# Kernel tuning notes

Hardware: AMD Instinct MI355X
Metric: run time of the kernel (lower is better)

Reference implementation:

```python
import jax, jax.numpy as jnp
import numpy as np

N, E, IN_C, HEADS, OUT_C = 50000, 800000, 256, 8, 32
NEG_SLOPE = 0.2
BN_EPS = 1e-5


def setup_inputs() -> dict:
    key = jax.random.key(0)
    ks = jax.random.split(key, 12)
    x = jax.random.normal(ks[0], (N, IN_C), jnp.float32)
    edge_index = jax.random.randint(ks[1], (2, E), 0, N, dtype=jnp.int32)
    edge_attr = jax.random.uniform(ks[2], (E, 1), jnp.float32)
    s = 0.1
    W = jax.random.normal(ks[3], (IN_C, HEADS * OUT_C), jnp.float32) * s
    att_src = jax.random.normal(ks[4], (HEADS, OUT_C), jnp.float32) * s
    att_dst = jax.random.normal(ks[5], (HEADS, OUT_C), jnp.float32) * s
    W_edge = jax.random.normal(ks[6], (1, HEADS * OUT_C), jnp.float32) * s
    att_edge = jax.random.normal(ks[7], (HEADS, OUT_C), jnp.float32) * s
    bias = jnp.zeros((HEADS * OUT_C,), jnp.float32)
    gamma = jnp.ones((HEADS * OUT_C,), jnp.float32)
    beta = jnp.zeros((HEADS * OUT_C,), jnp.float32)
    return {"x": x, "edge_index": edge_index, "edge_attr": edge_attr, "W": W,
            "att_src": att_src, "att_dst": att_dst, "W_edge": W_edge,
            "att_edge": att_edge, "bias": bias, "gamma": gamma, "beta": beta}


def reference(x, edge_index, edge_attr, W, att_src, att_dst, W_edge, att_edge, bias, gamma, beta):
    # --- add self loops (fill_value='mean' for edge_attr, PyG GATConv default) ---
    loops = jnp.arange(N, dtype=edge_index.dtype)
    src = jnp.concatenate([edge_index[0], loops])      # [E+N]
    dst = jnp.concatenate([edge_index[1], loops])      # [E+N]
    ea_mean = jnp.mean(edge_attr, axis=0, keepdims=True)
    ea = jnp.concatenate([edge_attr, jnp.broadcast_to(ea_mean, (N, edge_attr.shape[1]))], axis=0)

    # --- linear projections ---
    h = (x @ W).reshape(N, HEADS, OUT_C)               # [N,H,C]
    a_src = jnp.einsum('nhc,hc->nh', h, att_src)       # [N,H]
    a_dst = jnp.einsum('nhc,hc->nh', h, att_dst)       # [N,H]
    he = (ea @ W_edge).reshape(-1, HEADS, OUT_C)       # [E+N,H,C]
    a_edge = jnp.einsum('ehc,hc->eh', he, att_edge)    # [E+N,H]

    # --- edge-wise attention logits + segment softmax over destination nodes ---
    alpha = jax.nn.leaky_relu(a_src[src] + a_dst[dst] + a_edge, NEG_SLOPE)  # [E+N,H]
    amax = jax.ops.segment_max(alpha, dst, num_segments=N)  # every node has a self loop
    alpha = jnp.exp(alpha - amax[dst])
    asum = jax.ops.segment_sum(alpha, dst, num_segments=N)
    alpha = alpha / (asum[dst] + 1e-16)

    # --- weighted aggregation (attention dropout is identity in eval) ---
    msg = alpha[:, :, None] * h[src]                   # [E+N,H,C]
    out = jax.ops.segment_sum(msg, dst, num_segments=N).reshape(N, HEADS * OUT_C) + bias

    # --- BatchNorm (batch stats) + ELU; feature dropout is identity in eval ---
    mean = jnp.mean(out, axis=0)
    var = jnp.var(out, axis=0)
    out = (out - mean) * jax.lax.rsqrt(var + BN_EPS) * gamma + beta
    return jax.nn.elu(out)
```

## Files before the change

### kernel.cpp

```cpp
#include <hip/hip_runtime.h>
#include <hip/hip_bf16.h>
#include <math.h>

#define HEADS 8
#define OUTC 32
#define INC 256
#define OC 256
#define NEG_SLOPE 0.2f
#define BN_EPS 1e-5f
#define HS_STRIDE 264
#define CURP 16

typedef __attribute__((ext_vector_type(8))) short short8;
typedef __attribute__((ext_vector_type(4))) float floatx4;

__device__ __forceinline__ float bf2f(ushort u) {
    union { uint i; float f; } c; c.i = ((uint)u) << 16; return c.f;
}
__device__ __forceinline__ ushort f2bf(float f) {
    union { float f; uint i; } c; c.f = f;
    uint i = c.i + 0x7fffu + ((c.i >> 16) & 1u);
    return (ushort)(i >> 16);
}
__device__ __forceinline__ float loadf(const void* src, int t, uint flag) {
    return flag ? bf2f(((const ushort*)src)[t]) : ((const float*)src)[t];
}
__device__ __forceinline__ uint dtype_flag(const uint* gamma_raw) {
    return gamma_raw[0] != 0x3F800000u ? 1u : 0u;
}

__global__ void k_setup(const void* __restrict__ W, ushort* __restrict__ WT,
                        const void* __restrict__ att_src, const void* __restrict__ att_dst,
                        const void* __restrict__ gamma, const void* __restrict__ beta,
                        const void* __restrict__ We, const void* __restrict__ ae,
                        float* __restrict__ attS, float* __restrict__ attD,
                        float* __restrict__ gam, float* __restrict__ bet,
                        float* __restrict__ cvals, float* __restrict__ stats,
                        const void* __restrict__ eattr, const int* __restrict__ ei,
                        float* __restrict__ easum, int* __restrict__ deg, int E) {
    uint flag = dtype_flag((const uint*)gamma);
    int b = blockIdx.x, t = threadIdx.x;
    if (b < 256) {
        float v = loadf(W, b * OC + t, flag);
        WT[(size_t)t * INC + b] = f2bf(v);
    } else if (b == 256) {
        attS[t] = loadf(att_src, t, flag);
        attD[t] = loadf(att_dst, t, flag);
        gam[t]  = loadf(gamma, t, flag);
        bet[t]  = loadf(beta, t, flag);
        stats[t] = 0.f;
        stats[OC + t] = 0.f;
        __shared__ float s[OC];
        s[t] = loadf(We, t, flag) * loadf(ae, t, flag);
        __syncthreads();
        if (t < HEADS) {
            float v = 0.f;
            #pragma unroll
            for (int j = 0; j < OUTC; j++) v += s[t * OUTC + j];
            cvals[t] = v;
        }
    } else {
        int eb = b - 257;
        float v = 0.f;
        for (int i = eb * 256 + t; i < E; i += 512 * 256) {
            v += loadf(eattr, i, flag);
            atomicAdd(&deg[ei[E + i]], 1);
        }
        #pragma unroll
        for (int off = 32; off; off >>= 1) v += __shfl_down(v, off, 64);
        if ((t & 63) == 0) atomicAdd(easum, v);
    }
}

__global__ void __launch_bounds__(256, 2) k_gemm(const void* __restrict__ xraw,
                                                 const ushort* __restrict__ WT,
                                                 ushort* __restrict__ Hb,
                                                 const float* __restrict__ attS,
                                                 const float* __restrict__ attD,
                                                 float* __restrict__ asrc,
                                                 float* __restrict__ adst,
                                                 int N, const uint* __restrict__ graw) {
    uint flag = dtype_flag(graw);
    __shared__ ushort hs[2][16 * HS_STRIDE];
    __shared__ ushort hc[16 * HS_STRIDE];
    int wave = threadIdx.x >> 6;
    int lane = threadIdx.x & 63;
    int m = lane & 15, q = lane >> 4;

    short8 bfr[4][8];
    #pragma unroll
    for (int i = 0; i < 4; i++) {
        const short8* wb = (const short8*)(WT + (size_t)((wave * 4 + i) * 16 + m) * INC);
        #pragma unroll
        for (int kk = 0; kk < 8; kk++) bfr[i][kk] = wb[kk * 4 + q];
    }

    int ch0 = threadIdx.x * 2;
    int r0c = ch0 >> 5, seg0 = ch0 & 31;
    int r1c = (ch0 + 1) >> 5, seg1 = (ch0 + 1) & 31;

    auto loadA = [&](int row0, short8& v0, short8& v1) {
        #pragma unroll
        for (int c = 0; c < 2; c++) {
            int r = c ? r1c : r0c, seg = c ? seg1 : seg0;
            int row = row0 + r; if (row > N - 1) row = N - 1;
            short8 v;
            if (flag) {
                v = *(const short8*)((const ushort*)xraw + (size_t)row * INC + seg * 8);
            } else {
                const float4* xf = (const float4*)((const float*)xraw + (size_t)row * INC + seg * 8);
                float4 f0 = xf[0], f1 = xf[1];
                v[0] = (short)f2bf(f0.x); v[1] = (short)f2bf(f0.y);
                v[2] = (short)f2bf(f0.z); v[3] = (short)f2bf(f0.w);
                v[4] = (short)f2bf(f1.x); v[5] = (short)f2bf(f1.y);
                v[6] = (short)f2bf(f1.z); v[7] = (short)f2bf(f1.w);
            }
            if (c == 0) v0 = v; else v1 = v;
        }
    };

    int tiles = (N + 15) >> 4;
    const int GRID = gridDim.x;
    int rt = blockIdx.x;
    if (rt >= tiles) return;

    {
        short8 v0, v1;
        loadA(rt << 4, v0, v1);
        *(short8*)(&hs[0][r0c * HS_STRIDE + seg0 * 8]) = v0;
        *(short8*)(&hs[0][r1c * HS_STRIDE + seg1 * 8]) = v1;
    }
    __syncthreads();

    int cur = 0;
    while (true) {
        int row0 = rt << 4;
        int nrt = rt + GRID;
        bool hasnext = nrt < tiles;
        short8 nv0, nv1;
        if (hasnext) loadA(nrt << 4, nv0, nv1);
        short8 afr[8];
        #pragma unroll
        for (int kk = 0; kk < 8; kk++)
            afr[kk] = *(const short8*)(&hs[cur][m * HS_STRIDE + kk * 32 + q * 8]);
        floatx4 acc[4];
        #pragma unroll
        for (int i = 0; i < 4; i++) {
            floatx4 a = {0.f, 0.f, 0.f, 0.f};
            #pragma unroll
            for (int kk = 0; kk < 8; kk++)
                a = __builtin_amdgcn_mfma_f32_16x16x32_bf16(afr[kk], bfr[i][kk], a, 0, 0, 0);
            acc[i] = a;
        }
        __syncthreads();
        #pragma unroll
        for (int i = 0; i < 4; i++) {
            int col = (wave * 4 + i) * 16 + m;
            #pragma unroll
            for (int r4 = 0; r4 < 4; r4++)
                hc[(q * 4 + r4) * HS_STRIDE + col] = f2bf(acc[i][r4]);
        }
        if (hasnext) {
            *(short8*)(&hs[cur ^ 1][r0c * HS_STRIDE + seg0 * 8]) = nv0;
            *(short8*)(&hs[cur ^ 1][r1c * HS_STRIDE + seg1 * 8]) = nv1;
        }
        __syncthreads();
        #pragma unroll
        for (int c = 0; c < 2; c++) {
            int r = c ? r1c : r0c, seg = c ? seg1 : seg0;
            int row = row0 + r;
            if (row < N) {
                short8 v = *(const short8*)(&hc[r * HS_STRIDE + seg * 8]);
                *(short8*)(Hb + (size_t)row * OC + seg * 8) = v;
            }
        }
        {
            int half = threadIdx.x & 1;
            int hd = (threadIdx.x >> 1) & 7;
            int lr = threadIdx.x >> 4;
            int n = row0 + lr;
            const ushort4* hrow = (const ushort4*)(&hc[lr * HS_STRIDE + hd * OUTC]) + half * 4;
            const float* as = attS + hd * OUTC + half * 16;
            const float* ad = attD + hd * OUTC + half * 16;
            float s1 = 0.f, s2 = 0.f;
            #pragma unroll
            for (int c4 = 0; c4 < 4; c4++) {
                ushort4 u = hrow[c4];
                float v0 = bf2f(u.x), v1 = bf2f(u.y), v2 = bf2f(u.z), v3 = bf2f(u.w);
                s1 += v0 * as[c4*4+0] + v1 * as[c4*4+1] + v2 * as[c4*4+2] + v3 * as[c4*4+3];
                s2 += v0 * ad[c4*4+0] + v1 * ad[c4*4+1] + v2 * ad[c4*4+2] + v3 * ad[c4*4+3];
            }
            s1 += __shfl_xor(s1, 1, 64);
            s2 += __shfl_xor(s2, 1, 64);
            if (half == 0 && n < N) {
                asrc[n * HEADS + hd] = s1;
                adst[n * HEADS + hd] = s2;
            }
        }
        if (!hasnext) break;
        rt = nrt;
        cur ^= 1;
    }
}

__global__ void k_scan_local(const int* __restrict__ deg, int* __restrict__ part,
                             int* __restrict__ bsum, int N) {
    __shared__ int sth[256];
    int b = blockIdx.x, t = threadIdx.x;
    int base = b * 1024 + t * 4;
    int v0 = 0, v1 = 0, v2 = 0, v3 = 0;
    if (base + 0 < N) v0 = deg[base + 0] + 1;
    if (base + 1 < N) v1 = deg[base + 1] + 1;
    if (base + 2 < N) v2 = deg[base + 2] + 1;
    if (base + 3 < N) v3 = deg[base + 3] + 1;
    int tsum = v0 + v1 + v2 + v3;
    sth[t] = tsum;
    __syncthreads();
    #pragma unroll
    for (int off = 1; off < 256; off <<= 1) {
        int x = (t >= off) ? sth[t - off] : 0;
        __syncthreads();
        sth[t] += x;
        __syncthreads();
    }
    int excl = sth[t] - tsum;
    if (base + 0 < N) part[base + 0] = excl;
    if (base + 1 < N) part[base + 1] = excl + v0;
    if (base + 2 < N) part[base + 2] = excl + v0 + v1;
    if (base + 3 < N) part[base + 3] = excl + v0 + v1 + v2;
    if (t == 255) bsum[b] = sth[255];
}

__global__ void k_scan_blocks(const int* __restrict__ bsum, int* __restrict__ boff,
                              int nb, int* __restrict__ total) {
    __shared__ int sdata[256];
    __shared__ int carry;
    int t = threadIdx.x;
    if (t == 0) carry = 0;
    __syncthreads();
    for (int base = 0; base < nb; base += 256) {
        int v = (base + t < nb) ? bsum[base + t] : 0;
        sdata[t] = v;
        __syncthreads();
        #pragma unroll
        for (int off = 1; off < 256; off <<= 1) {
            int x = (t >= off) ? sdata[t - off] : 0;
            __syncthreads();
            sdata[t] += x;
            __syncthreads();
        }
        if (base + t < nb) boff[base + t] = carry + sdata[t] - v;
        __syncthreads();
        if (t == 255) carry += sdata[255];
        __syncthreads();
    }
    if (t == 0) total[0] = carry;
}

__global__ void k_scan_add(const int* __restrict__ part, const int* __restrict__ boff,
                           const int* __restrict__ total, int* __restrict__ rowstart,
                           int* __restrict__ cursor, int N) {
    int t = blockIdx.x * 256 + threadIdx.x;
    if (t < N) {
        int v = part[t] + boff[t >> 10];
        rowstart[t] = v;
        cursor[(size_t)t * CURP] = v;
    }
    if (t == 0) rowstart[N] = total[0];
}

__global__ void k_scatter(const int* __restrict__ ei, const void* __restrict__ eattr,
                          const float* __restrict__ easum, int* __restrict__ cursor,
                          uint* __restrict__ cpk, int E, int N,
                          const uint* __restrict__ graw) {
    uint flag = dtype_flag(graw);
    int t = blockIdx.x * 256 + threadIdx.x;
    if (t >= E + N) return;
    int s, d; float ea;
    if (t < E) { s = ei[t]; d = ei[E + t]; ea = loadf(eattr, t, flag); }
    else       { s = t - E; d = s;         ea = easum[0] / (float)E; }
    int pos = atomicAdd(&cursor[(size_t)d * CURP], 1);
    cpk[pos] = ((uint)f2bf(ea) << 16) | ((uint)s & 0xFFFFu);
}

__global__ void __launch_bounds__(256) k_aggf(const int* __restrict__ rowstart,
                                              const uint* __restrict__ cpk,
                                              const float* __restrict__ asrc,
                                              const float* __restrict__ adst,
                                              const float* __restrict__ cvals,
                                              const ushort* __restrict__ Hb,
                                              ushort* __restrict__ outpre, int N) {
    int d = blockIdx.x * 4 + (threadIdx.x >> 6);
    if (d >= N) return;
    int lane = threadIdx.x & 63;
    int hd = lane >> 3;
    float ad = adst[d * HEADS + hd];
    float ch = cvals[hd];
    int beg = __builtin_amdgcn_readfirstlane(rowstart[d]);
    int end = __builtin_amdgcn_readfirstlane(rowstart[d + 1]);
    int l8 = lane & 7;
    float4 acc = {0.f, 0.f, 0.f, 0.f};
    float psum = 0.f;
    int j = beg;
    for (; j + 8 <= end; j += 8) {
        uint epack = cpk[j + l8];
        int sk[8]; float eaf[8];
        #pragma unroll
        for (int k = 0; k < 8; k++) {
            uint e = (uint)__builtin_amdgcn_readlane((int)epack, k);
            sk[k] = (int)(e & 0xFFFFu);
            eaf[k] = bf2f((ushort)(e >> 16));
        }
        ushort4 u[8]; float a[8];
        #pragma unroll
        for (int k = 0; k < 8; k++)
            u[k] = *(const ushort4*)(Hb + (size_t)sk[k] * OC + lane * 4);
        #pragma unroll
        for (int k = 0; k < 8; k++)
            a[k] = asrc[sk[k] * HEADS + hd];
        #pragma unroll
        for (int k = 0; k < 8; k++) {
            float l = (a[k] + ad) + eaf[k] * ch;
            l = fmaxf(l, NEG_SLOPE * l);
            float pe = __expf(l);
            psum += pe;
            acc.x += pe * bf2f(u[k].x); acc.y += pe * bf2f(u[k].y);
            acc.z += pe * bf2f(u[k].z); acc.w += pe * bf2f(u[k].w);
        }
    }
    int rem = end - j;
    if (rem > 0) {
        int jj = j + l8; if (jj > end - 1) jj = end - 1;
        uint epack = cpk[jj];
        int sk[8]; float eaf[8];
        #pragma unroll
        for (int k = 0; k < 8; k++) {
            uint e = (uint)__builtin_amdgcn_readlane((int)epack, k);
            sk[k] = (int)(e & 0xFFFFu);
            eaf[k] = bf2f((ushort)(e >> 16));
        }
        ushort4 u[8]; float a[8];
        #pragma unroll
        for (int k = 0; k < 8; k++)
            u[k] = *(const ushort4*)(Hb + (size_t)sk[k] * OC + lane * 4);
        #pragma unroll
        for (int k = 0; k < 8; k++)
            a[k] = asrc[sk[k] * HEADS + hd];
        #pragma unroll
        for (int k = 0; k < 8; k++) {
            float l = (a[k] + ad) + eaf[k] * ch;
            l = fmaxf(l, NEG_SLOPE * l);
            float pe = (k < rem) ? __expf(l) : 0.f;
            psum += pe;
            acc.x += pe * bf2f(u[k].x); acc.y += pe * bf2f(u[k].y);
            acc.z += pe * bf2f(u[k].z); acc.w += pe * bf2f(u[k].w);
        }
    }
    float inv = 1.f / (psum + 1e-16f);
    ushort4 o;
    o.x = f2bf(acc.x * inv); o.y = f2bf(acc.y * inv);
    o.z = f2bf(acc.z * inv); o.w = f2bf(acc.w * inv);
    *(ushort4*)(outpre + (size_t)d * OC + lane * 4) = o;
}

__global__ void __launch_bounds__(256) k_bnstats(const ushort* __restrict__ outpre,
                                                 float* __restrict__ stats, int N) {
    int t = threadIdx.x;
    int lane = t & 63, rr = t >> 6;
    int f4 = lane * 4;
    float r1[4] = {0.f, 0.f, 0.f, 0.f};
    float r2[4] = {0.f, 0.f, 0.f, 0.f};
    for (int n0 = blockIdx.x * 16 + rr * 4; n0 < N; n0 += gridDim.x * 16) {
        ushort4 u[4];
        #pragma unroll
        for (int j = 0; j < 4; j++) {
            int n = n0 + j;
            ushort4 z = {0, 0, 0, 0};
            u[j] = (n < N) ? *(const ushort4*)(outpre + (size_t)n * OC + f4) : z;
        }
        #pragma unroll
        for (int j = 0; j < 4; j++) {
            float v0 = bf2f(u[j].x), v1 = bf2f(u[j].y), v2 = bf2f(u[j].z), v3 = bf2f(u[j].w);
            r1[0] += v0; r2[0] += v0 * v0;
            r1[1] += v1; r2[1] += v1 * v1;
            r1[2] += v2; r2[2] += v2 * v2;
            r1[3] += v3; r2[3] += v3 * v3;
        }
    }
    __shared__ float sred[8][256];
    float4 a1 = {r1[0], r1[1], r1[2], r1[3]};
    float4 a2 = {r2[0], r2[1], r2[2], r2[3]};
    *(float4*)&sred[rr][f4]     = a1;
    *(float4*)&sred[4 + rr][f4] = a2;
    __syncthreads();
    float s1 = sred[0][t] + sred[1][t] + sred[2][t] + sred[3][t];
    float s2 = sred[4][t] + sred[5][t] + sred[6][t] + sred[7][t];
    atomicAdd(&stats[t], s1);
    atomicAdd(&stats[OC + t], s2);
}

__global__ void __launch_bounds__(256) k_bnelu(const ushort* __restrict__ outpre,
                                               const float* __restrict__ stats,
                                               const float* __restrict__ gam,
                                               const float* __restrict__ bet,
                                               void* __restrict__ out, int N,
                                               const uint* __restrict__ graw) {
    uint flag = dtype_flag(graw);
    __shared__ float sc[OC], sh[OC];
    int t = threadIdx.x;
    {
        float invN = 1.f / (float)N;
        float mean = stats[t] * invN;
        float var  = stats[OC + t] * invN - mean * mean;
        float s = rsqrtf(var + BN_EPS) * gam[t];
        sc[t] = s;
        sh[t] = bet[t] - mean * s;
    }
    __syncthreads();
    int lane = t & 63, rr = t >> 6;
    int f4 = lane * 4;
    float s0 = sc[f4 + 0], s1 = sc[f4 + 1], s2 = sc[f4 + 2], s3 = sc[f4 + 3];
    float h0 = sh[f4 + 0], h1 = sh[f4 + 1], h2 = sh[f4 + 2], h3 = sh[f4 + 3];
    for (int n = blockIdx.x * 4 + rr; n < N; n += gridDim.x * 4) {
        ushort4 u = *(const ushort4*)(outpre + (size_t)n * OC + f4);
        float r0 = bf2f(u.x) * s0 + h0;
        float r1 = bf2f(u.y) * s1 + h1;
        float r2 = bf2f(u.z) * s2 + h2;
        float r3 = bf2f(u.w) * s3 + h3;
        r0 = r0 > 0.f ? r0 : expm1f(r0);
        r1 = r1 > 0.f ? r1 : expm1f(r1);
        r2 = r2 > 0.f ? r2 : expm1f(r2);
        r3 = r3 > 0.f ? r3 : expm1f(r3);
        if (flag) {
            ushort4 o; o.x = f2bf(r0); o.y = f2bf(r1); o.z = f2bf(r2); o.w = f2bf(r3);
            *(ushort4*)((ushort*)out + (size_t)n * OC + f4) = o;
        } else {
            float4 o; o.x = r0; o.y = r1; o.z = r2; o.w = r3;
            *(float4*)((float*)out + (size_t)n * OC + f4) = o;
        }
    }
}

extern "C" void kernel_launch(void* const* d_in, const int* in_sizes, int n_in,
                              void* d_out, int out_size, void* d_ws, size_t ws_size,
                              hipStream_t stream) {
    const void* x        = d_in[0];
    const int*  ei       = (const int*)d_in[1];
    const void* eattr    = d_in[2];
    const void* W        = d_in[3];
    const void* att_src  = d_in[4];
    const void* att_dst  = d_in[5];
    const void* W_edge   = d_in[6];
    const void* att_edge = d_in[7];
    const void* gamma    = d_in[9];
    const void* beta     = d_in[10];
    const uint* graw     = (const uint*)gamma;

    int N = in_sizes[0] / INC;
    int E = in_sizes[1] / 2;
    int T = E + N;
    int nb = (N + 1023) / 1024;

    char* ws = (char*)d_ws;
    size_t off = 0;
    auto alloc = [&](size_t bytes) -> void* {
        void* pp = ws + off;
        off += (bytes + 255) & ~(size_t)255;
        return pp;
    };
    ushort* WT       = (ushort*)alloc((size_t)INC * OC * 2);
    float*  attS     = (float*)alloc(OC * 4);
    float*  attD     = (float*)alloc(OC * 4);
    float*  gam      = (float*)alloc(OC * 4);
    float*  bet      = (float*)alloc(OC * 4);
    ushort* Hb       = (ushort*)alloc((size_t)N * OC * 2);
    float*  asrc     = (float*)alloc((size_t)N * HEADS * 4);
    float*  adst     = (float*)alloc((size_t)N * HEADS * 4);
    int*    deg      = (int*)alloc((size_t)N * 4);
    int*    part     = (int*)alloc((size_t)N * 4);
    int*    bsum     = (int*)alloc((size_t)(nb + 1) * 4);
    int*    boff     = (int*)alloc((size_t)(nb + 1) * 4);
    int*    total    = (int*)alloc(256);
    int*    rowstart = (int*)alloc((size_t)(N + 1) * 4);
    int*    cursor   = (int*)alloc((size_t)N * CURP * 4);
    uint*   cpk      = (uint*)alloc((size_t)T * 4);
    ushort* outpre   = (ushort*)alloc((size_t)N * OC * 2);
    float*  stats    = (float*)alloc(2 * OC * 4);
    float*  easum    = (float*)alloc(256);
    float*  cvals    = (float*)alloc(256);

    hipMemsetAsync(easum, 0, 4, stream);
    hipMemsetAsync(deg, 0, (size_t)N * 4, stream);

    k_setup<<<769, 256, 0, stream>>>(W, WT, att_src, att_dst, gamma, beta, W_edge,
                                     att_edge, attS, attD, gam, bet, cvals, stats,
                                     eattr, ei, easum, deg, E);

    k_scan_local<<<nb, 256, 0, stream>>>(deg, part, bsum, N);
    k_scan_blocks<<<1, 256, 0, stream>>>(bsum, boff, nb, total);
    k_scan_add<<<(N + 255) / 256, 256, 0, stream>>>(part, boff, total, rowstart, cursor, N);
    k_scatter<<<(T + 255) / 256, 256, 0, stream>>>(ei, eattr, easum, cursor, cpk, E, N, graw);

    int tiles = (N + 15) / 16;
    int gblocks = tiles < 1024 ? tiles : 1024;
    k_gemm<<<gblocks, 256, 0, stream>>>(x, WT, Hb, attS, attD, asrc, adst, N, graw);
    k_aggf<<<(N + 3) / 4, 256, 0, stream>>>(rowstart, cpk, asrc, adst, cvals, Hb, outpre, N);
    k_bnstats<<<512, 256, 0, stream>>>(outpre, stats, N);
    k_bnelu<<<512, 256, 0, stream>>>(outpre, stats, gam, bet, d_out, N, graw);
}
```

Baseline: 350.1 us.

## Fuse CSR scatter into GEMM launch via interleaved block roles

Merges the edge scatter kernel into the GEMM kernel by giving every third block the scatter role, a grid-stride loop over edges plus self loops, while the other blocks run the persistent MFMA GEMM with a fixed grid stride. The aim is to overlap the atomic-heavy, memory-bound scatter with the compute-bound projection and to save one kernel launch. In exchange the GEMM grid is now hardcoded to 1024 tiles of stride, and scatter blocks share CU resources with GEMM blocks (same LDS allocation declared), which may lower GEMM occupancy.

```diff
diff --git a/kernel.cpp b/kernel.cpp
--- a/kernel.cpp
+++ b/kernel.cpp
@@ -10,6 +10,8 @@
 #define BN_EPS 1e-5f
 #define HS_STRIDE 264
 #define CURP 16
+#define GEMM_GRID 1024
+#define SCAT_GRID 512
 
 typedef __attribute__((ext_vector_type(8))) short short8;
 typedef __attribute__((ext_vector_type(4))) float floatx4;
@@ -72,17 +74,105 @@
     }
 }
 
-__global__ void __launch_bounds__(256, 2) k_gemm(const void* __restrict__ xraw,
-                                                 const ushort* __restrict__ WT,
-                                                 ushort* __restrict__ Hb,
-                                                 const float* __restrict__ attS,
-                                                 const float* __restrict__ attD,
-                                                 float* __restrict__ asrc,
-                                                 float* __restrict__ adst,
-                                                 int N, const uint* __restrict__ graw) {
+__global__ void k_scan_local(const int* __restrict__ deg, int* __restrict__ part,
+                             int* __restrict__ bsum, int N) {
+    __shared__ int sth[256];
+    int b = blockIdx.x, t = threadIdx.x;
+    int base = b * 1024 + t * 4;
+    int v0 = 0, v1 = 0, v2 = 0, v3 = 0;
+    if (base + 0 < N) v0 = deg[base + 0] + 1;
+    if (base + 1 < N) v1 = deg[base + 1] + 1;
+    if (base + 2 < N) v2 = deg[base + 2] + 1;
+    if (base + 3 < N) v3 = deg[base + 3] + 1;
+    int tsum = v0 + v1 + v2 + v3;
+    sth[t] = tsum;
+    __syncthreads();
+    #pragma unroll
+    for (int off = 1; off < 256; off <<= 1) {
+        int x = (t >= off) ? sth[t - off] : 0;
+        __syncthreads();
+        sth[t] += x;
+        __syncthreads();
+    }
+    int excl = sth[t] - tsum;
+    if (base + 0 < N) part[base + 0] = excl;
+    if (base + 1 < N) part[base + 1] = excl + v0;
+    if (base + 2 < N) part[base + 2] = excl + v0 + v1;
+    if (base + 3 < N) part[base + 3] = excl + v0 + v1 + v2;
+    if (t == 255) bsum[b] = sth[255];
+}
+
+__global__ void k_scan_blocks(const int* __restrict__ bsum, int* __restrict__ boff,
+                              int nb, int* __restrict__ total) {
+    __shared__ int sdata[256];
+    __shared__ int carry;
+    int t = threadIdx.x;
+    if (t == 0) carry = 0;
+    __syncthreads();
+    for (int base = 0; base < nb; base += 256) {
+        int v = (base + t < nb) ? bsum[base + t] : 0;
+        sdata[t] = v;
+        __syncthreads();
+        #pragma unroll
+        for (int off = 1; off < 256; off <<= 1) {
+            int x = (t >= off) ? sdata[t - off] : 0;
+            __syncthreads();
+            sdata[t] += x;
+            __syncthreads();
+        }
+        if (base + t < nb) boff[base + t] = carry + sdata[t] - v;
+        __syncthreads();
+        if (t == 255) carry += sdata[255];
+        __syncthreads();
+    }
+    if (t == 0) total[0] = carry;
+}
+
+__global__ void k_scan_add(const int* __restrict__ part, const int* __restrict__ boff,
+                           const int* __restrict__ total, int* __restrict__ rowstart,
+                           int* __restrict__ cursor, int N) {
+    int t = blockIdx.x * 256 + threadIdx.x;
+    if (t < N) {
+        int v = part[t] + boff[t >> 10];
+        rowstart[t] = v;
+        cursor[(size_t)t * CURP] = v;
+    }
+    if (t == 0) rowstart[N] = total[0];
+}
+
+__global__ void __launch_bounds__(256, 2) k_gemmsc(const void* __restrict__ xraw,
+                                                   const ushort* __restrict__ WT,
+                                                   ushort* __restrict__ Hb,
+                                                   const float* __restrict__ attS,
+                                                   const float* __restrict__ attD,
+                                                   float* __restrict__ asrc,
+                                                   float* __restrict__ adst,
+                                                   const int* __restrict__ ei,
+                                                   const void* __restrict__ eattr,
+                                                   const float* __restrict__ easum,
+                                                   int* __restrict__ cursor,
+                                                   uint* __restrict__ cpk,
+                                                   int N, int E,
+                                                   const uint* __restrict__ graw) {
     uint flag = dtype_flag(graw);
     __shared__ ushort hs[2][16 * HS_STRIDE];
     __shared__ ushort hc[16 * HS_STRIDE];
+    int bid = blockIdx.x;
+
+    if (bid % 3 == 2) {
+        int sid = bid / 3;
+        int T = E + N;
+        for (int i = sid * 256 + threadIdx.x; i < T; i += SCAT_GRID * 256) {
+            int s, d; float ea;
+            if (i < E) { s = ei[i]; d = ei[E + i]; ea = loadf(eattr, i, flag); }
+            else       { s = i - E; d = s;         ea = easum[0] / (float)E; }
+            int pos = atomicAdd(&cursor[(size_t)d * CURP], 1);
+            cpk[pos] = ((uint)f2bf(ea) << 16) | ((uint)s & 0xFFFFu);
+        }
+        return;
+    }
+
+    int gid = (bid / 3) * 2 + (bid % 3);
     int wave = threadIdx.x >> 6;
     int lane = threadIdx.x & 63;
     int m = lane & 15, q = lane >> 4;
@@ -120,8 +210,7 @@
     };
 
     int tiles = (N + 15) >> 4;
-    const int GRID = gridDim.x;
-    int rt = blockIdx.x;
+    int rt = gid;
     if (rt >= tiles) return;
 
     {
@@ -135,7 +224,7 @@
     int cur = 0;
     while (true) {
         int row0 = rt << 4;
-        int nrt = rt + GRID;
+        int nrt = rt + GEMM_GRID;
         bool hasnext = nrt < tiles;
         short8 nv0, nv1;
         if (hasnext) loadA(nrt << 4, nv0, nv1);
@@ -203,86 +292,6 @@
     }
 }
 
-__global__ void k_scan_local(const int* __restrict__ deg, int* __restrict__ part,
-                             int* __restrict__ bsum, int N) {
-    __shared__ int sth[256];
-    int b = blockIdx.x, t = threadIdx.x;
-    int base = b * 1024 + t * 4;
-    int v0 = 0, v1 = 0, v2 = 0, v3 = 0;
-    if (base + 0 < N) v0 = deg[base + 0] + 1;
-    if (base + 1 < N) v1 = deg[base + 1] + 1;
-    if (base + 2 < N) v2 = deg[base + 2] + 1;
-    if (base + 3 < N) v3 = deg[base + 3] + 1;
-    int tsum = v0 + v1 + v2 + v3;
-    sth[t] = tsum;
-    __syncthreads();
-    #pragma unroll
-    for (int off = 1; off < 256; off <<= 1) {
-        int x = (t >= off) ? sth[t - off] : 0;
-        __syncthreads();
-        sth[t] += x;
-        __syncthreads();
-    }
-    int excl = sth[t] - tsum;
-    if (base + 0 < N) part[base + 0] = excl;
-    if (base + 1 < N) part[base + 1] = excl + v0;
-    if (base + 2 < N) part[base + 2] = excl + v0 + v1;
-    if (base + 3 < N) part[base + 3] = excl + v0 + v1 + v2;
-    if (t == 255) bsum[b] = sth[255];
-}
-
-__global__ void k_scan_blocks(const int* __restrict__ bsum, int* __restrict__ boff,
-                              int nb, int* __restrict__ total) {
-    __shared__ int sdata[256];
-    __shared__ int carry;
-    int t = threadIdx.x;
-    if (t == 0) carry = 0;
-    __syncthreads();
-    for (int base = 0; base < nb; base += 256) {
-        int v = (base + t < nb) ? bsum[base + t] : 0;
-        sdata[t] = v;
-        __syncthreads();
-        #pragma unroll
-        for (int off = 1; off < 256; off <<= 1) {
-            int x = (t >= off) ? sdata[t - off] : 0;
-            __syncthreads();
-            sdata[t] += x;
-            __syncthreads();
-        }
-        if (base + t < nb) boff[base + t] = carry + sdata[t] - v;
-        __syncthreads();
-        if (t == 255) carry += sdata[255];
-        __syncthreads();
-    }
-    if (t == 0) total[0] = carry;
-}
-
-__global__ void k_scan_add(const int* __restrict__ part, const int* __restrict__ boff,
-                           const int* __restrict__ total, int* __restrict__ rowstart,
-                           int* __restrict__ cursor, int N) {
-    int t = blockIdx.x * 256 + threadIdx.x;
-    if (t < N) {
-        int v = part[t] + boff[t >> 10];
-        rowstart[t] = v;
-        cursor[(size_t)t * CURP] = v;
-    }
-    if (t == 0) rowstart[N] = total[0];
-}
-
-__global__ void k_scatter(const int* __restrict__ ei, const void* __restrict__ eattr,
-                          const float* __restrict__ easum, int* __restrict__ cursor,
-                          uint* __restrict__ cpk, int E, int N,
-                          const uint* __restrict__ graw) {
-    uint flag = dtype_flag(graw);
-    int t = blockIdx.x * 256 + threadIdx.x;
-    if (t >= E + N) return;
-    int s, d; float ea;
-    if (t < E) { s = ei[t]; d = ei[E + t]; ea = loadf(eattr, t, flag); }
-    else       { s = t - E; d = s;         ea = easum[0] / (float)E; }
-    int pos = atomicAdd(&cursor[(size_t)d * CURP], 1);
-    cpk[pos] = ((uint)f2bf(ea) << 16) | ((uint)s & 0xFFFFu);
-}
-
 __global__ void __launch_bounds__(256) k_aggf(const int* __restrict__ rowstart,
                                               const uint* __restrict__ cpk,
                                               const float* __restrict__ asrc,
@@ -458,7 +467,6 @@
 
     int N = in_sizes[0] / INC;
     int E = in_sizes[1] / 2;
-    int T = E + N;
     int nb = (N + 1023) / 1024;
 
     char* ws = (char*)d_ws;
@@ -483,7 +491,7 @@
     int*    total    = (int*)alloc(256);
     int*    rowstart = (int*)alloc((size_t)(N + 1) * 4);
     int*    cursor   = (int*)alloc((size_t)N * CURP * 4);
-    uint*   cpk      = (uint*)alloc((size_t)T * 4);
+    uint*   cpk      = (uint*)alloc((size_t)(E + N) * 4);
     ushort* outpre   = (ushort*)alloc((size_t)N * OC * 2);
     float*  stats    = (float*)alloc(2 * OC * 4);
     float*  easum    = (float*)alloc(256);
@@ -499,11 +507,11 @@
     k_scan_local<<<nb, 256, 0, stream>>>(deg, part, bsum, N);
     k_scan_blocks<<<1, 256, 0, stream>>>(bsum, boff, nb, total);
     k_scan_add<<<(N + 255) / 256, 256, 0, stream>>>(part, boff, total, rowstart, cursor, N);
-    k_scatter<<<(T + 255) / 256, 256, 0, stream>>>(ei, eattr, easum, cursor, cpk, E, N, graw);
-
-    int tiles = (N + 15) / 16;
-    int gblocks = tiles < 1024 ? tiles : 1024;
-    k_gemm<<<gblocks, 256, 0, stream>>>(x, WT, Hb, attS, attD, asrc, adst, N, graw);
+
+    k_gemmsc<<<GEMM_GRID + SCAT_GRID, 256, 0, stream>>>(x, WT, Hb, attS, attD, asrc,
+                                                        adst, ei, eattr, easum, cursor,
+                                                        cpk, N, E, graw);
+
     k_aggf<<<(N + 3) / 4, 256, 0, stream>>>(rowstart, cpk, asrc, adst, cvals, Hb, outpre, N);
     k_bnstats<<<512, 256, 0, stream>>>(outpre, stats, N);
     k_bnelu<<<512, 256, 0, stream>>>(outpre, stats, gam, bet, d_out, N, graw);
```

Measured after the change: 326.0 us. 1.07x faster.
